# Kernel tuning notes

Measured on AMD Instinct MI355X. Metric: run time of the kernel, lower is better.

## Reference

```python
import jax, jax.numpy as jnp
import numpy as np

E, B, T = 7, 50, 100               # ensemble (network_size), no_batches=50, time blocks
D, A, L, H, C = 128, 32, 256, 1024, 128  # data, action, latent, hidden, context sizes
H_STEP = 0.1                        # (t1 - t0) / T == dt -> one SDE step per block


def setup_inputs() -> dict:
    key = jax.random.key(0)
    ks = iter(jax.random.split(key, 64))
    def nrm(shape, scale=1.0):
        return jax.random.normal(next(ks), shape, jnp.float32) * scale
    def ens(i, o):
        s = 1.0 / np.sqrt(i)
        return nrm((E, i, o), s), nrm((E, o), s)
    def lin(i, o):
        s = 1.0 / np.sqrt(i)
        return nrm((i, o), s), nrm((o,), s)
    inp = {}
    inp["enc_w1"], inp["enc_b1"] = ens(D, H)
    inp["enc_w2"], inp["enc_b2"] = ens(H, H)
    inp["enc_w3"], inp["enc_b3"] = ens(H, C)
    inp["qz0_w"], inp["qz0_b"] = ens(C, 2 * L)
    inp["act_w"], inp["act_b"] = ens(L + A + D, L)
    inp["proj_w1"], inp["proj_b1"] = ens(L, H)
    inp["proj_w2"], inp["proj_b2"] = ens(H, H)
    inp["proj_w3"], inp["proj_b3"] = ens(H, D)
    inp["f_w1"], inp["f_b1"] = lin(L, H)
    inp["f_w2"], inp["f_b2"] = lin(H, H)
    inp["f_w3"], inp["f_b3"] = lin(H, L)
    inp["h_w1"], inp["h_b1"] = lin(L, H)
    inp["h_w2"], inp["h_b2"] = lin(H, H)
    inp["h_w3"], inp["h_b3"] = lin(H, L)
    # per-latent-dim g nets: Linear(1,H) -> ReLU -> Linear(H,1), stacked over L dims
    inp["g_w1"] = nrm((L, H), 0.2)
    inp["g_b1"] = nrm((L, H), 0.2)
    inp["g_w2"] = nrm((L, H), 0.2 / np.sqrt(H))
    inp["g_b2"] = 0.5 + nrm((L,), 0.01)   # keep diffusion bounded away from 0
    inp["pz0_mean"] = jnp.zeros((E, 1, L), jnp.float32)
    inp["pz0_logstd"] = jnp.zeros((E, 1, L), jnp.float32)
    inp["xs"] = nrm((E, T * B, D))
    inp["actions"] = nrm((E, T * B, A))
    inp["eps_z0"] = nrm((T, E, B, L))      # torch.randn_like noise for z0 reparam
    inp["dw_noise"] = nrm((T, E * B, L))   # Brownian increment noise (unit std)
    return inp


def reference(enc_w1, enc_b1, enc_w2, enc_b2, enc_w3, enc_b3,
              qz0_w, qz0_b, act_w, act_b,
              proj_w1, proj_b1, proj_w2, proj_b2, proj_w3, proj_b3,
              f_w1, f_b1, f_w2, f_b2, f_w3, f_b3,
              h_w1, h_b1, h_w2, h_b2, h_w3, h_b3,
              g_w1, g_b1, g_w2, g_b2,
              pz0_mean, pz0_logstd,
              xs, actions, eps_z0, dw_noise):
    def ens_lin(x, w, b):  # EnsembleFC: bmm + bias
        return jnp.einsum('ebi,eio->ebo', x, w) + b[:, None, :]

    def encoder(x):
        x = jax.nn.relu(ens_lin(x, enc_w1, enc_b1))
        x = jax.nn.relu(ens_lin(x, enc_w2, enc_b2))
        return ens_lin(x, enc_w3, enc_b3)

    def projector(z):
        z = jnp.tanh(ens_lin(z, proj_w1, proj_b1))
        z = jnp.tanh(ens_lin(z, proj_w2, proj_b2))
        return ens_lin(z, proj_w3, proj_b3)

    def mlp(y, w1, b1, w2, b2, w3, b3):  # Linear-ReLU-Linear-Tanh-Linear
        y = jax.nn.relu(y @ w1 + b1)
        y = jnp.tanh(y @ w2 + b2)
        return y @ w3 + b3

    def g_fn(y):  # vectorized per-dim tiny MLPs: y (N, L) -> (N, L)
        hh = jax.nn.relu(y[:, :, None] * g_w1[None] + g_b1[None])  # (N, L, H)
        return jnp.sum(hh * g_w2[None], axis=-1) + g_b2

    xs_t = jnp.moveaxis(xs.reshape(E, T, B, D), 1, 0)        # (T, E, B, D)
    act_t = jnp.moveaxis(actions.reshape(E, T, B, A), 1, 0)  # (T, E, B, A)
    sqrt_h = jnp.sqrt(jnp.float32(H_STEP))

    def step(carry, inps):
        zs_last, i = carry
        x_i, a_i, eps_i, dw_i = inps
        ctx = encoder(x_i)                                  # (E, B, C)
        q = ens_lin(ctx, qz0_w, qz0_b)                      # (E, B, 2L)
        qm, ql = q[..., :L], q[..., L:]
        z0 = qm + jnp.exp(ql) * eps_i
        z_in = jnp.where(i == 0, z0, zs_last)               # first step uses z0
        lad = jnp.concatenate([z_in, a_i, x_i], axis=2)
        z = ens_lin(lad, act_w, act_b).reshape(E * B, L)
        # one SDE step with logqp (f: posterior drift, h: prior drift, g: diffusion)
        fv = mlp(z, f_w1, f_b1, f_w2, f_b2, f_w3, f_b3)
        hv = mlp(z, h_w1, h_b1, h_w2, h_b2, h_w3, h_b3)
        gv = g_fn(z)
        u = (fv - hv) / gv
        lr = 0.5 * jnp.sum(u * u, axis=-1) * H_STEP         # (E*B,) log-ratio increment
        z_new = z + fv * H_STEP + gv * (sqrt_h * dw_i)
        zs_new = z_new.reshape(E, B, L)
        xm = projector(zs_new)                              # (E, B, D)
        # KL(q(z0) || p(z0)) for diagonal Gaussians
        kl = (pz0_logstd - ql) \
             + (jnp.exp(2.0 * ql) + (qm - pz0_mean) ** 2) / (2.0 * jnp.exp(2.0 * pz0_logstd)) \
             - 0.5
        logqp0 = kl.sum(axis=2).mean(axis=1)                # (E,)
        lr_mean = lr.reshape(E, B).mean(axis=1)             # (E,)
        return (zs_new, i + 1), (lr_mean, logqp0, xm)

    init = (jnp.zeros((E, B, L), xs.dtype), jnp.int32(0))
    (_, _), (lrm, lq0, xms) = jax.lax.scan(step, init, (xs_t, act_t, eps_z0, dw_noise))
    logqp_path = lrm.sum(axis=0) + lq0.sum(axis=0)          # (E,)
    predicted_xs = jnp.moveaxis(xms, 0, 1).reshape(E, T * B, D)
    return logqp_path, predicted_xs
```

## Files before the change

kernel.cpp:

```cpp
#include <hip/hip_runtime.h>
#include <hip/hip_bf16.h>
#include <math.h>

#define E_ 7
#define B_ 50
#define T_ 100
#define D_ 128
#define A_ 32
#define L_ 256
#define H_ 1024
#define C_ 128
#define LAD_ 416
#define EB_ 350
#define TB_ 5000
#define SQRTH 0.31622776601683794f

typedef __attribute__((ext_vector_type(8))) short s8v;
typedef __attribute__((ext_vector_type(4))) float f32x4;
typedef __hip_bfloat16 bf16;

struct BG {
  const bf16* A[8];
  const bf16* W[8];
  const float* bias[8];
  float* Cf[8];
  bf16* Cb[8];
};

template<int BM, int ACT, int OUT>
__global__ __launch_bounds__(256)
void bgemm(BG g, int M, int K, int lda, int ldw, int ldc) {
  __shared__ short As[BM * 64];
  __shared__ short Ws[128 * 64];
  const short* Ap = (const short*)g.A[blockIdx.z];
  const short* Wp = (const short*)g.W[blockIdx.z];
  const int bm = blockIdx.x * BM, bn = blockIdx.y * 128;
  const int tid = threadIdx.x;
  const int wv = tid >> 6, lane = tid & 63;
  const int wm0 = (wv >> 1) * (BM / 2), wn0 = (wv & 1) * 64;
  const int l15 = lane & 15, l4 = lane >> 4;
  constexpr int FM = BM / 32;
  constexpr int AI = BM / 32;
  f32x4 acc[FM][4] = {};
  for (int k0 = 0; k0 < K; k0 += 64) {
    s8v av[AI], wvv[4];
#pragma unroll
    for (int i = 0; i < AI; ++i) {
      const int c = tid + i * 256, r = c >> 3, ck = c & 7;
      s8v v = {};
      if (bm + r < M) v = *(const s8v*)(Ap + (size_t)(bm + r) * lda + k0 + ck * 8);
      av[i] = v;
    }
#pragma unroll
    for (int i = 0; i < 4; ++i) {
      const int c = tid + i * 256, r = c >> 3, ck = c & 7;
      wvv[i] = *(const s8v*)(Wp + (size_t)(bn + r) * ldw + k0 + ck * 8);
    }
    __syncthreads();
#pragma unroll
    for (int i = 0; i < AI; ++i) {
      const int c = tid + i * 256, r = c >> 3, ck = c & 7;
      *(s8v*)(As + r * 64 + ((ck ^ (r & 7)) << 3)) = av[i];
    }
#pragma unroll
    for (int i = 0; i < 4; ++i) {
      const int c = tid + i * 256, r = c >> 3, ck = c & 7;
      *(s8v*)(Ws + r * 64 + ((ck ^ (r & 7)) << 3)) = wvv[i];
    }
    __syncthreads();
#pragma unroll
    for (int ks = 0; ks < 2; ++ks) {
      s8v af[FM], bfr[4];
#pragma unroll
      for (int m = 0; m < FM; ++m) {
        const int r = wm0 + m * 16 + l15, ck = ks * 4 + l4;
        af[m] = *(const s8v*)(As + r * 64 + ((ck ^ (r & 7)) << 3));
      }
#pragma unroll
      for (int n = 0; n < 4; ++n) {
        const int r = wn0 + n * 16 + l15, ck = ks * 4 + l4;
        bfr[n] = *(const s8v*)(Ws + r * 64 + ((ck ^ (r & 7)) << 3));
      }
#pragma unroll
      for (int m = 0; m < FM; ++m)
#pragma unroll
        for (int n = 0; n < 4; ++n)
          acc[m][n] = __builtin_amdgcn_mfma_f32_16x16x32_bf16(af[m], bfr[n], acc[m][n], 0, 0, 0);
    }
    __syncthreads();
  }
  const float* bias = g.bias[blockIdx.z];
  float* Cf = g.Cf[blockIdx.z];
  bf16* Cb = g.Cb[blockIdx.z];
#pragma unroll
  for (int n = 0; n < 4; ++n) {
    const int col = bn + wn0 + n * 16 + l15;
    const float bv = bias ? bias[col] : 0.f;
#pragma unroll
    for (int m = 0; m < FM; ++m) {
#pragma unroll
      for (int j = 0; j < 4; ++j) {
        const int row = bm + wm0 + m * 16 + l4 * 4 + j;
        if (row < M) {
          float v = acc[m][n][j] + bv;
          if (ACT == 1) v = fmaxf(v, 0.f);
          if (ACT == 2) v = tanhf(v);
          if (OUT == 0) Cf[(size_t)row * ldc + col] = v;
          if (OUT == 1) Cb[(size_t)row * ldc + col] = __float2bfloat16(v);
        }
      }
    }
  }
}

__global__ __launch_bounds__(256)
void cvtT_kernel(const float* __restrict__ src, bf16* __restrict__ dst,
                 int K, int N, long ss, long ds) {
  __shared__ float t[32][33];
  src += (size_t)blockIdx.z * ss;
  dst += (size_t)blockIdx.z * ds;
  const int n0 = blockIdx.x * 32, k0 = blockIdx.y * 32;
  const int tx = threadIdx.x & 31, ty = threadIdx.x >> 5;
#pragma unroll
  for (int i = 0; i < 4; ++i)
    t[ty + 8 * i][tx] = src[(size_t)(k0 + ty + 8 * i) * N + n0 + tx];
  __syncthreads();
#pragma unroll
  for (int i = 0; i < 4; ++i)
    dst[(size_t)(n0 + ty + 8 * i) * K + k0 + tx] = __float2bfloat16(t[tx][ty + 8 * i]);
}

struct B4 { bf16 a, b, c, d; };
__global__ __launch_bounds__(256)
void cvt_kernel(const float* __restrict__ s, bf16* __restrict__ d, int n4) {
  const int i = blockIdx.x * 256 + threadIdx.x;
  if (i < n4) {
    const float4 v = ((const float4*)s)[i];
    B4 o = {__float2bfloat16(v.x), __float2bfloat16(v.y),
            __float2bfloat16(v.z), __float2bfloat16(v.w)};
    ((B4*)d)[i] = o;
  }
}

__global__ __launch_bounds__(256)
void act_gemm(const float* __restrict__ zin, int zin_estride,
              const float* __restrict__ actions, const float* __restrict__ xs,
              const float* __restrict__ act_w, const float* __restrict__ act_b,
              float* __restrict__ zout, bf16* __restrict__ zout_bf, int t) {
  __shared__ float As[16][68];
  __shared__ float Bs[16][64];
  const int tid = threadIdx.x;
  const int e = blockIdx.y;
  const int bn = blockIdx.x * 64;
  const int tm = (tid >> 4) << 2;
  const int tn = (tid & 15) << 2;
  const int am = tid >> 2;
  const int ak = (tid & 3) << 2;
  const int bk = tid >> 4;
  const int bn4 = (tid & 15) << 2;
  const float* W = act_w + (size_t)e * LAD_ * L_;
  const float* zin_e = zin + (size_t)e * zin_estride;
  float acc[4][4] = {};
  for (int k0 = 0; k0 < LAD_; k0 += 16) {
    float4 av = make_float4(0.f, 0.f, 0.f, 0.f);
    const int k = k0 + ak;
    if (am < B_) {
      if (k < L_)
        av = *(const float4*)(zin_e + (size_t)am * L_ + k);
      else if (k < L_ + A_)
        av = *(const float4*)(actions + ((size_t)e * TB_ + (size_t)t * B_ + am) * A_ + (k - L_));
      else
        av = *(const float4*)(xs + ((size_t)e * TB_ + (size_t)t * B_ + am) * D_ + (k - L_ - A_));
    }
    const float4 wv = *(const float4*)(W + (size_t)(k0 + bk) * L_ + (bn + bn4));
    __syncthreads();
    As[ak + 0][am] = av.x; As[ak + 1][am] = av.y;
    As[ak + 2][am] = av.z; As[ak + 3][am] = av.w;
    *(float4*)&Bs[bk][bn4] = wv;
    __syncthreads();
#pragma unroll
    for (int kk = 0; kk < 16; ++kk) {
      const float4 a4 = *(const float4*)&As[kk][tm];
      const float4 b4 = *(const float4*)&Bs[kk][tn];
      const float ar[4] = {a4.x, a4.y, a4.z, a4.w};
      const float br[4] = {b4.x, b4.y, b4.z, b4.w};
#pragma unroll
      for (int i = 0; i < 4; ++i)
#pragma unroll
        for (int j = 0; j < 4; ++j)
          acc[i][j] = fmaf(ar[i], br[j], acc[i][j]);
    }
  }
#pragma unroll
  for (int i = 0; i < 4; ++i) {
    const int m = tm + i;
    if (m < B_) {
#pragma unroll
      for (int j = 0; j < 4; ++j) {
        const float v = acc[i][j] + act_b[(size_t)e * L_ + bn + tn + j];
        const size_t idx = ((size_t)e * B_ + m) * L_ + (bn + tn + j);
        zout[idx] = v;
        zout_bf[idx] = __float2bfloat16(v);
      }
    }
  }
}

__global__ __launch_bounds__(256)
void qkl_kernel(const float* __restrict__ ctx, int rows, int row_off, int ctx_estride,
                const float* __restrict__ qw, const float* __restrict__ qb,
                const float* __restrict__ pm, const float* __restrict__ pl,
                const float* __restrict__ eps0, float* __restrict__ z0,
                float* __restrict__ logqp) {
  __shared__ float cx[16][128];
  __shared__ float red[16];
  const int e = blockIdx.y;
  const int r0 = blockIdx.x * 16;
  const int tid = threadIdx.x;
  {
    const int r = tid >> 4, c = (tid & 15) * 8;
    float4 v0 = make_float4(0.f, 0.f, 0.f, 0.f), v1 = v0;
    if (r0 + r < rows) {
      const float* src = ctx + (size_t)e * ctx_estride + (size_t)(r0 + r) * C_ + c;
      v0 = *(const float4*)src;
      v1 = *(const float4*)(src + 4);
    }
    *(float4*)&cx[r][c] = v0;
    *(float4*)&cx[r][c + 4] = v1;
  }
  if (tid < 16) red[tid] = 0.f;
  __syncthreads();
  const int j = tid;
  const float* w = qw + (size_t)e * C_ * 512;
  float am_[16] = {};
  float al_[16] = {};
  for (int k0 = 0; k0 < C_; k0 += 4) {
    float wm[4], wl[4];
#pragma unroll
    for (int q = 0; q < 4; ++q) {
      wm[q] = w[(size_t)(k0 + q) * 512 + j];
      wl[q] = w[(size_t)(k0 + q) * 512 + 256 + j];
    }
#pragma unroll
    for (int r = 0; r < 16; ++r) {
      const float4 cv = *(const float4*)&cx[r][k0];
      const float cc[4] = {cv.x, cv.y, cv.z, cv.w};
#pragma unroll
      for (int q = 0; q < 4; ++q) {
        am_[r] = fmaf(cc[q], wm[q], am_[r]);
        al_[r] = fmaf(cc[q], wl[q], al_[r]);
      }
    }
  }
  const float qbm = qb[(size_t)e * 512 + j];
  const float qbl = qb[(size_t)e * 512 + 256 + j];
  const float pmv = pm[(size_t)e * L_ + j];
  const float plv = pl[(size_t)e * L_ + j];
  const float inv2e = 0.5f * expf(-2.f * plv);
#pragma unroll
  for (int r = 0; r < 16; ++r) {
    float kl = 0.f;
    if (r0 + r < rows) {
      const float qm_ = am_[r] + qbm;
      const float ql_ = al_[r] + qbl;
      const float dm = qm_ - pmv;
      kl = plv - ql_ + (expf(2.f * ql_) + dm * dm) * inv2e - 0.5f;
      const int gi = row_off + r0 + r;
      if (gi < B_) {
        const size_t zi = ((size_t)e * B_ + gi) * L_ + j;
        z0[zi] = qm_ + expf(ql_) * eps0[zi];
      }
    }
    for (int off = 32; off; off >>= 1) kl += __shfl_xor(kl, off, 64);
    if ((tid & 63) == 0) atomicAdd(&red[r], kl);
  }
  __syncthreads();
  if (tid < 16 && r0 + tid < rows) atomicAdd(&logqp[e], red[tid] * (1.0f / B_));
}

__global__ __launch_bounds__(64)
void g_kernel(const float* __restrict__ z, const float* __restrict__ gw1,
              const float* __restrict__ gb1, const float* __restrict__ gw2,
              const float* __restrict__ gb2, float* __restrict__ gv) {
  const int l = blockIdx.x;
  const int r0 = blockIdx.y * 44;
  const int rend = (r0 + 44 < EB_) ? (r0 + 44) : EB_;
  const int lane = threadIdx.x;
  float w1[16], b1[16], w2[16];
#pragma unroll
  for (int i = 0; i < 16; ++i) {
    const int h = lane + i * 64;
    w1[i] = gw1[(size_t)l * H_ + h];
    b1[i] = gb1[(size_t)l * H_ + h];
    w2[i] = gw2[(size_t)l * H_ + h];
  }
  const float g2 = gb2[l];
  for (int r = r0; r < rend; ++r) {
    const float zv = z[(size_t)r * L_ + l];
    float acc = 0.f;
#pragma unroll
    for (int i = 0; i < 16; ++i) {
      float hh = fmaf(zv, w1[i], b1[i]);
      hh = fmaxf(hh, 0.f);
      acc = fmaf(hh, w2[i], acc);
    }
    for (int off = 32; off; off >>= 1) acc += __shfl_xor(acc, off, 64);
    if (lane == 0) gv[(size_t)r * L_ + l] = acc + g2;
  }
}

__global__ __launch_bounds__(256)
void epi_kernel(const float* __restrict__ fvp, const float* __restrict__ fb3,
                const float* __restrict__ hb3, const float* __restrict__ gv,
                const float* __restrict__ z, const float* __restrict__ dw,
                float* __restrict__ zs_all, bf16* __restrict__ zs_bf,
                float* __restrict__ logqp, int t) {
  __shared__ float wsum[4];
  const int r = blockIdx.x;
  const int l = threadIdx.x;
  const int e = r / B_, b = r - e * B_;
  const size_t rl = (size_t)r * L_ + l;
  float fv = fb3[l], hv = hb3[l];
#pragma unroll
  for (int s = 0; s < 4; ++s) {
    fv += fvp[(size_t)s * EB_ * L_ + rl];
    hv += fvp[(size_t)(4 + s) * EB_ * L_ + rl];
  }
  const float gvv = gv[rl];
  const float u = (fv - hv) / gvv;
  float s_ = u * u;
  for (int off = 32; off; off >>= 1) s_ += __shfl_xor(s_, off, 64);
  if ((l & 63) == 0) wsum[l >> 6] = s_;
  __syncthreads();
  if (l == 0) {
    const float tot = wsum[0] + wsum[1] + wsum[2] + wsum[3];
    atomicAdd(&logqp[e], 0.5f * tot * 0.1f * (1.0f / B_));
  }
  const float znew = z[rl] + fv * 0.1f + gvv * (SQRTH * dw[(size_t)t * EB_ * L_ + rl]);
  const size_t oi = (((size_t)e * T_ + t) * B_ + b) * L_ + l;
  zs_all[oi] = znew;
  zs_bf[oi] = __float2bfloat16(znew);
}

__global__ void init_kernel(float* logqp) {
  if (threadIdx.x < E_) logqp[threadIdx.x] = 0.f;
}

extern "C" void kernel_launch(void* const* d_in, const int* in_sizes, int n_in,
                              void* d_out, int out_size, void* d_ws, size_t ws_size,
                              hipStream_t stream) {
  (void)in_sizes; (void)n_in; (void)out_size;
  const float* enc_w1 = (const float*)d_in[0];
  const float* enc_b1 = (const float*)d_in[1];
  const float* enc_w2 = (const float*)d_in[2];
  const float* enc_b2 = (const float*)d_in[3];
  const float* enc_w3 = (const float*)d_in[4];
  const float* enc_b3 = (const float*)d_in[5];
  const float* qz0_w  = (const float*)d_in[6];
  const float* qz0_b  = (const float*)d_in[7];
  const float* act_w  = (const float*)d_in[8];
  const float* act_b  = (const float*)d_in[9];
  const float* proj_w1 = (const float*)d_in[10];
  const float* proj_b1 = (const float*)d_in[11];
  const float* proj_w2 = (const float*)d_in[12];
  const float* proj_b2 = (const float*)d_in[13];
  const float* proj_w3 = (const float*)d_in[14];
  const float* proj_b3 = (const float*)d_in[15];
  const float* f_w1 = (const float*)d_in[16];
  const float* f_b1 = (const float*)d_in[17];
  const float* f_w2 = (const float*)d_in[18];
  const float* f_b2 = (const float*)d_in[19];
  const float* f_w3 = (const float*)d_in[20];
  const float* f_b3 = (const float*)d_in[21];
  const float* h_w1 = (const float*)d_in[22];
  const float* h_b1 = (const float*)d_in[23];
  const float* h_w2 = (const float*)d_in[24];
  const float* h_b2 = (const float*)d_in[25];
  const float* h_w3 = (const float*)d_in[26];
  const float* h_b3 = (const float*)d_in[27];
  const float* g_w1 = (const float*)d_in[28];
  const float* g_b1 = (const float*)d_in[29];
  const float* g_w2 = (const float*)d_in[30];
  const float* g_b2 = (const float*)d_in[31];
  const float* pz0_mean   = (const float*)d_in[32];
  const float* pz0_logstd = (const float*)d_in[33];
  const float* xs      = (const float*)d_in[34];
  const float* actions = (const float*)d_in[35];
  const float* eps_z0  = (const float*)d_in[36];
  const float* dw      = (const float*)d_in[37];

  float* out = (float*)d_out;
  float* logqp = out;
  float* pred = out + E_;

  char* base = (char*)d_ws;
  size_t off = 0;
  auto alloc = [&](size_t bytes) {
    void* p = base + off;
    off = (off + bytes + 255) & ~(size_t)255;
    return p;
  };
  float* zs_all = (float*)alloc((size_t)E_ * T_ * B_ * L_ * 4);
  bf16* zs_bf   = (bf16*)alloc((size_t)E_ * T_ * B_ * L_ * 2);
  float* z0     = (float*)alloc((size_t)E_ * B_ * L_ * 4);
  float* zbuf   = (float*)alloc((size_t)EB_ * L_ * 4);
  bf16* zbuf_bf = (bf16*)alloc((size_t)EB_ * L_ * 2);
  bf16* fh1     = (bf16*)alloc((size_t)2 * EB_ * H_ * 2);
  bf16* fh2     = (bf16*)alloc((size_t)2 * EB_ * H_ * 2);
  float* fvhvp  = (float*)alloc((size_t)8 * EB_ * L_ * 4);
  float* gvb    = (float*)alloc((size_t)EB_ * L_ * 4);
  bf16* xs_bf   = (bf16*)alloc((size_t)E_ * TB_ * D_ * 2);
  bf16* ew1T = (bf16*)alloc((size_t)E_ * D_ * H_ * 2);
  bf16* ew2T = (bf16*)alloc((size_t)E_ * H_ * H_ * 2);
  bf16* ew3T = (bf16*)alloc((size_t)E_ * H_ * C_ * 2);
  bf16* pw1T = (bf16*)alloc((size_t)E_ * L_ * H_ * 2);
  bf16* pw2T = (bf16*)alloc((size_t)E_ * H_ * H_ * 2);
  bf16* pw3T = (bf16*)alloc((size_t)E_ * H_ * D_ * 2);
  bf16* fw1T = (bf16*)alloc((size_t)L_ * H_ * 2);
  bf16* fw2T = (bf16*)alloc((size_t)H_ * H_ * 2);
  bf16* fw3T = (bf16*)alloc((size_t)H_ * L_ * 2);
  bf16* hw1T = (bf16*)alloc((size_t)L_ * H_ * 2);
  bf16* hw2T = (bf16*)alloc((size_t)H_ * H_ * 2);
  bf16* hw3T = (bf16*)alloc((size_t)H_ * L_ * 2);
  const size_t per_row = (size_t)E_ * (H_ * 2 * 2 + C_ * 4);
  size_t remain = (ws_size > off + 4096) ? (ws_size - off - 4096) : 0;
  int CH = (int)(remain / per_row);
  if (CH > 2500) CH = 2500;
  if (CH < 64) CH = 64;
  bf16* bufA = (bf16*)alloc((size_t)E_ * CH * H_ * 2);
  bf16* bufB = (bf16*)alloc((size_t)E_ * CH * H_ * 2);
  float* bufC = (float*)alloc((size_t)E_ * CH * C_ * 4);

  init_kernel<<<dim3(1), dim3(64), 0, stream>>>(logqp);

  const dim3 cb(256);
  cvt_kernel<<<dim3((E_ * TB_ * D_ / 4 + 255) / 256), cb, 0, stream>>>(xs, xs_bf, E_ * TB_ * D_ / 4);
  cvtT_kernel<<<dim3(H_ / 32, D_ / 32, E_), cb, 0, stream>>>(enc_w1, ew1T, D_, H_, (long)D_ * H_, (long)D_ * H_);
  cvtT_kernel<<<dim3(H_ / 32, H_ / 32, E_), cb, 0, stream>>>(enc_w2, ew2T, H_, H_, (long)H_ * H_, (long)H_ * H_);
  cvtT_kernel<<<dim3(C_ / 32, H_ / 32, E_), cb, 0, stream>>>(enc_w3, ew3T, H_, C_, (long)H_ * C_, (long)H_ * C_);
  cvtT_kernel<<<dim3(H_ / 32, L_ / 32, E_), cb, 0, stream>>>(proj_w1, pw1T, L_, H_, (long)L_ * H_, (long)L_ * H_);
  cvtT_kernel<<<dim3(H_ / 32, H_ / 32, E_), cb, 0, stream>>>(proj_w2, pw2T, H_, H_, (long)H_ * H_, (long)H_ * H_);
  cvtT_kernel<<<dim3(D_ / 32, H_ / 32, E_), cb, 0, stream>>>(proj_w3, pw3T, H_, D_, (long)H_ * D_, (long)H_ * D_);
  cvtT_kernel<<<dim3(H_ / 32, L_ / 32, 1), cb, 0, stream>>>(f_w1, fw1T, L_, H_, 0, 0);
  cvtT_kernel<<<dim3(H_ / 32, H_ / 32, 1), cb, 0, stream>>>(f_w2, fw2T, H_, H_, 0, 0);
  cvtT_kernel<<<dim3(L_ / 32, H_ / 32, 1), cb, 0, stream>>>(f_w3, fw3T, H_, L_, 0, 0);
  cvtT_kernel<<<dim3(H_ / 32, L_ / 32, 1), cb, 0, stream>>>(h_w1, hw1T, L_, H_, 0, 0);
  cvtT_kernel<<<dim3(H_ / 32, H_ / 32, 1), cb, 0, stream>>>(h_w2, hw2T, H_, H_, 0, 0);
  cvtT_kernel<<<dim3(L_ / 32, H_ / 32, 1), cb, 0, stream>>>(h_w3, hw3T, H_, L_, 0, 0);

  BG g;
  for (int c = 0; c < TB_; c += CH) {
    const int rows = (TB_ - c < CH) ? (TB_ - c) : CH;
    const int mt = (rows + 127) / 128;
    for (int e = 0; e < E_; ++e) {
      g.A[e] = xs_bf + ((size_t)e * TB_ + c) * D_;
      g.W[e] = ew1T + (size_t)e * D_ * H_;
      g.bias[e] = enc_b1 + (size_t)e * H_;
      g.Cb[e] = bufA + (size_t)e * CH * H_;
    }
    bgemm<128, 1, 1><<<dim3(mt, H_ / 128, E_), 256, 0, stream>>>(g, rows, D_, D_, D_, H_);
    for (int e = 0; e < E_; ++e) {
      g.A[e] = bufA + (size_t)e * CH * H_;
      g.W[e] = ew2T + (size_t)e * H_ * H_;
      g.bias[e] = enc_b2 + (size_t)e * H_;
      g.Cb[e] = bufB + (size_t)e * CH * H_;
    }
    bgemm<128, 1, 1><<<dim3(mt, H_ / 128, E_), 256, 0, stream>>>(g, rows, H_, H_, H_, H_);
    for (int e = 0; e < E_; ++e) {
      g.A[e] = bufB + (size_t)e * CH * H_;
      g.W[e] = ew3T + (size_t)e * H_ * C_;
      g.bias[e] = enc_b3 + (size_t)e * C_;
      g.Cf[e] = bufC + (size_t)e * CH * C_;
    }
    bgemm<128, 0, 0><<<dim3(mt, C_ / 128, E_), 256, 0, stream>>>(g, rows, H_, H_, H_, C_);
    qkl_kernel<<<dim3((rows + 15) / 16, E_), 256, 0, stream>>>(
        bufC, rows, c, CH * C_, qz0_w, qz0_b, pz0_mean, pz0_logstd, eps_z0, z0, logqp);
  }

  for (int t = 0; t < T_; ++t) {
    const float* zin;
    int zes;
    if (t == 0) { zin = z0; zes = B_ * L_; }
    else { zin = zs_all + (size_t)(t - 1) * B_ * L_; zes = T_ * B_ * L_; }
    act_gemm<<<dim3(L_ / 64, E_), 256, 0, stream>>>(zin, zes, actions, xs, act_w, act_b,
                                                    zbuf, zbuf_bf, t);
    g.A[0] = zbuf_bf; g.W[0] = fw1T; g.bias[0] = f_b1; g.Cb[0] = fh1;
    g.A[1] = zbuf_bf; g.W[1] = hw1T; g.bias[1] = h_b1; g.Cb[1] = fh1 + (size_t)EB_ * H_;
    bgemm<64, 1, 1><<<dim3(6, H_ / 128, 2), 256, 0, stream>>>(g, EB_, L_, L_, L_, H_);
    g.A[0] = fh1; g.W[0] = fw2T; g.bias[0] = f_b2; g.Cb[0] = fh2;
    g.A[1] = fh1 + (size_t)EB_ * H_; g.W[1] = hw2T; g.bias[1] = h_b2;
    g.Cb[1] = fh2 + (size_t)EB_ * H_;
    bgemm<64, 2, 1><<<dim3(6, H_ / 128, 2), 256, 0, stream>>>(g, EB_, H_, H_, H_, H_);
    for (int jj = 0; jj < 8; ++jj) {
      const int fb = jj >> 2, s = jj & 3;
      g.A[jj] = fh2 + (size_t)fb * EB_ * H_ + s * 256;
      g.W[jj] = (fb ? hw3T : fw3T) + s * 256;
      g.bias[jj] = nullptr;
      g.Cf[jj] = fvhvp + (size_t)jj * EB_ * L_;
    }
    bgemm<64, 0, 0><<<dim3(6, L_ / 128, 8), 256, 0, stream>>>(g, EB_, 256, H_, H_, L_);
    g_kernel<<<dim3(L_, 8), 64, 0, stream>>>(zbuf, g_w1, g_b1, g_w2, g_b2, gvb);
    epi_kernel<<<dim3(EB_), 256, 0, stream>>>(fvhvp, f_b3, h_b3, gvb, zbuf, dw,
                                              zs_all, zs_bf, logqp, t);
  }

  for (int c = 0; c < TB_; c += CH) {
    const int rows = (TB_ - c < CH) ? (TB_ - c) : CH;
    const int mt = (rows + 127) / 128;
    for (int e = 0; e < E_; ++e) {
      g.A[e] = zs_bf + ((size_t)e * T_ * B_ + c) * L_;
      g.W[e] = pw1T + (size_t)e * L_ * H_;
      g.bias[e] = proj_b1 + (size_t)e * H_;
      g.Cb[e] = bufA + (size_t)e * CH * H_;
    }
    bgemm<128, 2, 1><<<dim3(mt, H_ / 128, E_), 256, 0, stream>>>(g, rows, L_, L_, L_, H_);
    for (int e = 0; e < E_; ++e) {
      g.A[e] = bufA + (size_t)e * CH * H_;
      g.W[e] = pw2T + (size_t)e * H_ * H_;
      g.bias[e] = proj_b2 + (size_t)e * H_;
      g.Cb[e] = bufB + (size_t)e * CH * H_;
    }
    bgemm<128, 2, 1><<<dim3(mt, H_ / 128, E_), 256, 0, stream>>>(g, rows, H_, H_, H_, H_);
    for (int e = 0; e < E_; ++e) {
      g.A[e] = bufB + (size_t)e * CH * H_;
      g.W[e] = pw3T + (size_t)e * H_ * D_;
      g.bias[e] = proj_b3 + (size_t)e * D_;
      g.Cf[e] = pred + ((size_t)e * TB_ + c) * D_;
    }
    bgemm<128, 0, 0><<<dim3(mt, D_ / 128, E_), 256, 0, stream>>>(g, rows, H_, H_, H_, D_);
  }
}
```

Before: 11.16 ms.

## Fuse the 100-step SDE scan into one persistent kernel with grid barriers

```diff
diff --git a/kernel.cpp b/kernel.cpp
--- a/kernel.cpp
+++ b/kernel.cpp
@@ -10,14 +10,19 @@
 #define L_ 256
 #define H_ 1024
 #define C_ 128
-#define LAD_ 416
 #define EB_ 350
 #define TB_ 5000
 #define SQRTH 0.31622776601683794f
+#define NWG 512
+#define RPAD 352
+#define ZPAD 368
 
 typedef __attribute__((ext_vector_type(8))) short s8v;
 typedef __attribute__((ext_vector_type(4))) float f32x4;
+typedef _Float16 f16x2 __attribute__((ext_vector_type(2)));
 typedef __hip_bfloat16 bf16;
+
+#define MFMA __builtin_amdgcn_mfma_f32_16x16x32_bf16
 
 struct BG {
   const bf16* A[8];
@@ -85,7 +90,7 @@
       for (int m = 0; m < FM; ++m)
 #pragma unroll
         for (int n = 0; n < 4; ++n)
-          acc[m][n] = __builtin_amdgcn_mfma_f32_16x16x32_bf16(af[m], bfr[n], acc[m][n], 0, 0, 0);
+          acc[m][n] = MFMA(af[m], bfr[n], acc[m][n], 0, 0, 0);
     }
     __syncthreads();
   }
@@ -143,75 +148,60 @@
 }
 
 __global__ __launch_bounds__(256)
-void act_gemm(const float* __restrict__ zin, int zin_estride,
-              const float* __restrict__ actions, const float* __restrict__ xs,
-              const float* __restrict__ act_w, const float* __restrict__ act_b,
-              float* __restrict__ zout, bf16* __restrict__ zout_bf, int t) {
-  __shared__ float As[16][68];
-  __shared__ float Bs[16][64];
-  const int tid = threadIdx.x;
-  const int e = blockIdx.y;
-  const int bn = blockIdx.x * 64;
-  const int tm = (tid >> 4) << 2;
-  const int tn = (tid & 15) << 2;
-  const int am = tid >> 2;
-  const int ak = (tid & 3) << 2;
-  const int bk = tid >> 4;
-  const int bn4 = (tid & 15) << 2;
-  const float* W = act_w + (size_t)e * LAD_ * L_;
-  const float* zin_e = zin + (size_t)e * zin_estride;
-  float acc[4][4] = {};
-  for (int k0 = 0; k0 < LAD_; k0 += 16) {
-    float4 av = make_float4(0.f, 0.f, 0.f, 0.f);
-    const int k = k0 + ak;
-    if (am < B_) {
-      if (k < L_)
-        av = *(const float4*)(zin_e + (size_t)am * L_ + k);
-      else if (k < L_ + A_)
-        av = *(const float4*)(actions + ((size_t)e * TB_ + (size_t)t * B_ + am) * A_ + (k - L_));
-      else
-        av = *(const float4*)(xs + ((size_t)e * TB_ + (size_t)t * B_ + am) * D_ + (k - L_ - A_));
-    }
-    const float4 wv = *(const float4*)(W + (size_t)(k0 + bk) * L_ + (bn + bn4));
-    __syncthreads();
-    As[ak + 0][am] = av.x; As[ak + 1][am] = av.y;
-    As[ak + 2][am] = av.z; As[ak + 3][am] = av.w;
-    *(float4*)&Bs[bk][bn4] = wv;
-    __syncthreads();
-#pragma unroll
-    for (int kk = 0; kk < 16; ++kk) {
-      const float4 a4 = *(const float4*)&As[kk][tm];
-      const float4 b4 = *(const float4*)&Bs[kk][tn];
-      const float ar[4] = {a4.x, a4.y, a4.z, a4.w};
-      const float br[4] = {b4.x, b4.y, b4.z, b4.w};
-#pragma unroll
-      for (int i = 0; i < 4; ++i)
-#pragma unroll
-        for (int j = 0; j < 4; ++j)
-          acc[i][j] = fmaf(ar[i], br[j], acc[i][j]);
-    }
-  }
-#pragma unroll
-  for (int i = 0; i < 4; ++i) {
-    const int m = tm + i;
-    if (m < B_) {
-#pragma unroll
-      for (int j = 0; j < 4; ++j) {
-        const float v = acc[i][j] + act_b[(size_t)e * L_ + bn + tn + j];
-        const size_t idx = ((size_t)e * B_ + m) * L_ + (bn + tn + j);
-        zout[idx] = v;
-        zout_bf[idx] = __float2bfloat16(v);
-      }
-    }
-  }
+void ax_build(const float* __restrict__ actions, const float* __restrict__ xs,
+              bf16* __restrict__ dst) {
+  const int idx = blockIdx.x * 256 + threadIdx.x;
+  if (idx >= E_ * TB_ * 192) return;
+  const int k = idx % 192;
+  const int r = (idx / 192) % TB_;
+  const int e = idx / (192 * TB_);
+  float v = 0.f;
+  if (k < 32) v = actions[((size_t)e * TB_ + r) * A_ + k];
+  else if (k < 160) v = xs[((size_t)e * TB_ + r) * D_ + (k - 32)];
+  dst[idx] = __float2bfloat16(v);
+}
+
+__global__ __launch_bounds__(256)
+void waxT_build(const float* __restrict__ act_w, bf16* __restrict__ dst) {
+  const int idx = blockIdx.x * 256 + threadIdx.x;
+  if (idx >= E_ * 256 * 192) return;
+  const int k = idx % 192;
+  const int n = (idx / 192) % 256;
+  const int e = idx / (192 * 256);
+  float v = (k < 160) ? act_w[(size_t)e * 416 * 256 + (size_t)(256 + k) * 256 + n] : 0.f;
+  dst[idx] = __float2bfloat16(v);
+}
+
+__global__ __launch_bounds__(256)
+void wsplitT_build(const float* __restrict__ act_w, bf16* __restrict__ hi,
+                   bf16* __restrict__ lo) {
+  const int idx = blockIdx.x * 256 + threadIdx.x;
+  if (idx >= E_ * 256 * 256) return;
+  const int k = idx & 255;
+  const int n = (idx >> 8) & 255;
+  const int e = idx >> 16;
+  const float w = act_w[(size_t)e * 416 * 256 + (size_t)k * 256 + n];
+  const bf16 h = __float2bfloat16(w);
+  hi[idx] = h;
+  lo[idx] = __float2bfloat16(w - __bfloat162float(h));
+}
+
+__global__ __launch_bounds__(256)
+void gpack_build(const float* __restrict__ gw1, const float* __restrict__ gb1,
+                 const float* __restrict__ gw2, _Float16* __restrict__ dst) {
+  const int idx = blockIdx.x * 256 + threadIdx.x;
+  if (idx >= 256 * 3 * 1024) return;
+  const int l = idx / 3072, rem = idx - l * 3072, arr = rem >> 10, h = rem & 1023;
+  const float* s = arr == 0 ? gw1 : (arr == 1 ? gb1 : gw2);
+  dst[idx] = (_Float16)s[(size_t)l * 1024 + h];
 }
 
 __global__ __launch_bounds__(256)
 void qkl_kernel(const float* __restrict__ ctx, int rows, int row_off, int ctx_estride,
                 const float* __restrict__ qw, const float* __restrict__ qb,
                 const float* __restrict__ pm, const float* __restrict__ pl,
-                const float* __restrict__ eps0, float* __restrict__ z0,
-                float* __restrict__ logqp) {
+                const float* __restrict__ eps0, bf16* __restrict__ z0hi,
+                bf16* __restrict__ z0lo, float* __restrict__ logqp) {
   __shared__ float cx[16][128];
   __shared__ float red[16];
   const int e = blockIdx.y;
@@ -268,7 +258,10 @@
       const int gi = row_off + r0 + r;
       if (gi < B_) {
         const size_t zi = ((size_t)e * B_ + gi) * L_ + j;
-        z0[zi] = qm_ + expf(ql_) * eps0[zi];
+        const float z0 = qm_ + expf(ql_) * eps0[zi];
+        const bf16 h = __float2bfloat16(z0);
+        z0hi[zi] = h;
+        z0lo[zi] = __float2bfloat16(z0 - __bfloat162float(h));
       }
     }
     for (int off = 32; off; off >>= 1) kl += __shfl_xor(kl, off, 64);
@@ -278,72 +271,356 @@
   if (tid < 16 && r0 + tid < rows) atomicAdd(&logqp[e], red[tid] * (1.0f / B_));
 }
 
-__global__ __launch_bounds__(64)
-void g_kernel(const float* __restrict__ z, const float* __restrict__ gw1,
-              const float* __restrict__ gb1, const float* __restrict__ gw2,
-              const float* __restrict__ gb2, float* __restrict__ gv) {
-  const int l = blockIdx.x;
-  const int r0 = blockIdx.y * 44;
-  const int rend = (r0 + 44 < EB_) ? (r0 + 44) : EB_;
-  const int lane = threadIdx.x;
-  float w1[16], b1[16], w2[16];
-#pragma unroll
-  for (int i = 0; i < 16; ++i) {
-    const int h = lane + i * 64;
-    w1[i] = gw1[(size_t)l * H_ + h];
-    b1[i] = gb1[(size_t)l * H_ + h];
-    w2[i] = gw2[(size_t)l * H_ + h];
-  }
-  const float g2 = gb2[l];
-  for (int r = r0; r < rend; ++r) {
-    const float zv = z[(size_t)r * L_ + l];
-    float acc = 0.f;
-#pragma unroll
-    for (int i = 0; i < 16; ++i) {
-      float hh = fmaf(zv, w1[i], b1[i]);
-      hh = fmaxf(hh, 0.f);
-      acc = fmaf(hh, w2[i], acc);
-    }
-    for (int off = 32; off; off >>= 1) acc += __shfl_xor(acc, off, 64);
-    if (lane == 0) gv[(size_t)r * L_ + l] = acc + g2;
-  }
-}
-
-__global__ __launch_bounds__(256)
-void epi_kernel(const float* __restrict__ fvp, const float* __restrict__ fb3,
-                const float* __restrict__ hb3, const float* __restrict__ gv,
-                const float* __restrict__ z, const float* __restrict__ dw,
-                float* __restrict__ zs_all, bf16* __restrict__ zs_bf,
-                float* __restrict__ logqp, int t) {
-  __shared__ float wsum[4];
-  const int r = blockIdx.x;
-  const int l = threadIdx.x;
-  const int e = r / B_, b = r - e * B_;
-  const size_t rl = (size_t)r * L_ + l;
-  float fv = fb3[l], hv = hb3[l];
-#pragma unroll
-  for (int s = 0; s < 4; ++s) {
-    fv += fvp[(size_t)s * EB_ * L_ + rl];
-    hv += fvp[(size_t)(4 + s) * EB_ * L_ + rl];
-  }
-  const float gvv = gv[rl];
-  const float u = (fv - hv) / gvv;
-  float s_ = u * u;
-  for (int off = 32; off; off >>= 1) s_ += __shfl_xor(s_, off, 64);
-  if ((l & 63) == 0) wsum[l >> 6] = s_;
+struct SA {
+  bf16 *zhi, *zlo;
+  float *zP, *zPT;
+  bf16 *zPb;
+  bf16 *fh1, *fh2;
+  float *fv, *hv, *gv;
+  const float* axw;
+  const bf16 *WzhiT, *WzloT;
+  const bf16 *fw1T, *hw1T, *fw2T, *hw2T, *fw3T, *hw3T;
+  const float *fb1, *hb1, *fb2, *hb2, *fb3, *hb3;
+  const _Float16* gf16;
+  const float* gb2;
+  const float* dw;
+  float* logqp;
+  bf16* zs_bf;
+  unsigned* bar;
+};
+
+__device__ __forceinline__ void gsync(unsigned* bar, unsigned ph, int tid, int wg) {
+  __threadfence();
   __syncthreads();
-  if (l == 0) {
-    const float tot = wsum[0] + wsum[1] + wsum[2] + wsum[3];
-    atomicAdd(&logqp[e], 0.5f * tot * 0.1f * (1.0f / B_));
-  }
-  const float znew = z[rl] + fv * 0.1f + gvv * (SQRTH * dw[(size_t)t * EB_ * L_ + rl]);
-  const size_t oi = (((size_t)e * T_ + t) * B_ + b) * L_ + l;
-  zs_all[oi] = znew;
-  zs_bf[oi] = __float2bfloat16(znew);
-}
-
-__global__ void init_kernel(float* logqp) {
-  if (threadIdx.x < E_) logqp[threadIdx.x] = 0.f;
+  if (tid == 0) {
+    const unsigned v = __hip_atomic_fetch_add(&bar[(wg >> 4) << 5], 1u,
+                                              __ATOMIC_RELAXED, __HIP_MEMORY_SCOPE_AGENT);
+    if (v + 1u == ph * 16u) {
+      const unsigned r = __hip_atomic_fetch_add(&bar[1024], 1u,
+                                                __ATOMIC_RELAXED, __HIP_MEMORY_SCOPE_AGENT);
+      if (r + 1u == ph * 32u)
+        __hip_atomic_store(&bar[1056], ph, __ATOMIC_RELAXED, __HIP_MEMORY_SCOPE_AGENT);
+    }
+    while (__hip_atomic_load(&bar[1056], __ATOMIC_RELAXED, __HIP_MEMORY_SCOPE_AGENT) < ph)
+      __builtin_amdgcn_s_sleep(4);
+  }
+  __syncthreads();
+  __threadfence();
+}
+
+__device__ __forceinline__ f16x2 relu2(f16x2 t) {
+#if __has_builtin(__builtin_elementwise_max)
+  const f16x2 zz = {};
+  return __builtin_elementwise_max(t, zz);
+#else
+  t[0] = t[0] > (_Float16)0 ? t[0] : (_Float16)0;
+  t[1] = t[1] > (_Float16)0 ? t[1] : (_Float16)0;
+  return t;
+#endif
+}
+__device__ __forceinline__ float fdot2a(f16x2 a, f16x2 b, float c) {
+#if __has_builtin(__builtin_amdgcn_fdot2)
+  return __builtin_amdgcn_fdot2(a, b, c, false);
+#else
+  return c + (float)a[0] * (float)b[0] + (float)a[1] * (float)b[1];
+#endif
+}
+
+__device__ void g_part(const SA& a, const f16x2* gwh, int wb, int l, float gb2v,
+                       int lane, int rb, int re) {
+  const int r0 = rb + lane, r1 = rb + 64 + lane;
+  const float z0f = (r0 < re) ? a.zPT[(size_t)l * RPAD + r0] : 0.f;
+  const float z1f = (r1 < re) ? a.zPT[(size_t)l * RPAD + r1] : 0.f;
+  const _Float16 z0h = (_Float16)z0f, z1h = (_Float16)z1f;
+  const f16x2 z20 = {z0h, z0h}, z21 = {z1h, z1h};
+  float ac0 = 0.f, ac1 = 0.f;
+  for (int hp = 0; hp < 512; ++hp) {
+    const f16x2 w1v = gwh[wb + hp];
+    const f16x2 b1v = gwh[wb + 512 + hp];
+    const f16x2 w2v = gwh[wb + 1024 + hp];
+    ac0 = fdot2a(relu2(z20 * w1v + b1v), w2v, ac0);
+    ac1 = fdot2a(relu2(z21 * w1v + b1v), w2v, ac1);
+  }
+  if (r0 < re) a.gv[(size_t)r0 * 256 + l] = ac0 + gb2v;
+  if (r1 < re) a.gv[(size_t)r1 * 256 + l] = ac1 + gb2v;
+}
+
+__global__ __launch_bounds__(256, 2) void scan_kernel(SA a) {
+  __shared__ __align__(16) char smem[32768];
+  short* sw = (short*)smem;
+  const int wg = blockIdx.x, tid = threadIdx.x;
+  const int lane = tid & 63, wv = tid >> 6, l15 = lane & 15, l4 = lane >> 4;
+
+  const bool isWZ = wg < 56;
+  const bool isW1 = wg >= 56 && wg < 120;
+  const bool isW2 = wg >= 120 && wg < 376;
+  const bool isW3 = wg >= 376 && wg < 440;
+  const bool isG  = wg >= 440 && wg < 504;
+
+  if (isWZ) {
+    const int e = wg >> 3, c0 = (wg & 7) * 32;
+    const short* gh = (const short*)a.WzhiT + ((size_t)e * 256 + c0) * 256;
+    const short* gl = (const short*)a.WzloT + ((size_t)e * 256 + c0) * 256;
+#pragma unroll
+    for (int i = 0; i < 4; ++i) {
+      const int lin = tid + i * 256;
+      const int col = lin >> 5, c = lin & 31;
+      const int dst = col * 256 + ((c ^ (col & 7)) << 3);
+      *(s8v*)(sw + dst) = *(const s8v*)(gh + col * 256 + c * 8);
+      *(s8v*)(sw + 8192 + dst) = *(const s8v*)(gl + col * 256 + c * 8);
+    }
+  } else if (isW1) {
+    const int idx = wg - 56, fb = idx >> 5, r5 = idx & 31;
+    const int n0 = (r5 >> 1) * 64;
+    const short* gsrc = (const short*)(fb ? a.hw1T : a.fw1T) + (size_t)n0 * 256;
+#pragma unroll
+    for (int i = 0; i < 8; ++i) {
+      const int lin = tid + i * 256;
+      const int col = lin >> 5, c = lin & 31;
+      *(s8v*)(sw + col * 256 + ((c ^ (col & 7)) << 3)) = *(const s8v*)(gsrc + col * 256 + c * 8);
+    }
+  } else if (isW2 || isW3) {
+    int n0, fb;
+    const bf16* base;
+    if (isW2) {
+      const int idx = wg - 120; fb = idx >> 7;
+      n0 = ((idx & 127) >> 1) * 16;
+      base = fb ? a.hw2T : a.fw2T;
+    } else {
+      const int idx = wg - 376; fb = idx >> 5;
+      n0 = ((idx & 31) >> 1) * 16;
+      base = fb ? a.hw3T : a.fw3T;
+    }
+    const short* gsrc = (const short*)base + (size_t)n0 * 1024;
+#pragma unroll
+    for (int i = 0; i < 8; ++i) {
+      const int lin = tid + i * 256;
+      const int col = lin >> 7, c = lin & 127;
+      *(s8v*)(sw + col * 1024 + ((c ^ (col & 7)) << 3)) = *(const s8v*)(gsrc + col * 1024 + c * 8);
+    }
+  } else if (isG) {
+    const unsigned* src = (const unsigned*)a.gf16 + (size_t)(wg - 440) * 4 * 1536;
+    unsigned* dstu = (unsigned*)smem;
+    for (int i = tid; i < 6144; i += 256) dstu[i] = src[i];
+  }
+  __syncthreads();
+
+  const f16x2* gwh = (const f16x2*)smem;
+  const int gl_ = isG ? (wg - 440) * 4 + wv : 0;
+  const float gb2v = isG ? a.gb2[gl_] : 0.f;
+  const int gwb = wv * 1536;
+
+  const int idx5 = wg * 256 + tid;
+  const bool act5 = idx5 < EB_ * 256;
+  const int r5i = idx5 >> 8, l5i = idx5 & 255;
+  const int e5 = act5 ? r5i / 50 : 0;
+  const int b5 = r5i - e5 * 50;
+  const size_t zsb = ((size_t)e5 * T_ * B_ + b5) * 256 + l5i;
+  float lr_acc = 0.f;
+  unsigned ph = 0;
+
+  for (int t = 0; t < T_; ++t) {
+    if (isWZ) {
+      const int e = wg >> 3, c0 = (wg & 7) * 32;
+      const int arow = e * 50 + wv * 16 + l15;
+      const short* zh = (const short*)a.zhi;
+      const short* zl = (const short*)a.zlo;
+      f32x4 acc[2] = {};
+#pragma unroll
+      for (int k0 = 0; k0 < 256; k0 += 32) {
+        const s8v ah = *(const s8v*)(zh + arow * 256 + k0 + l4 * 8);
+        const s8v al = *(const s8v*)(zl + arow * 256 + k0 + l4 * 8);
+        const int c = (k0 >> 3) + l4;
+#pragma unroll
+        for (int nt = 0; nt < 2; ++nt) {
+          const int cl = nt * 16 + l15;
+          const int off = cl * 256 + ((c ^ (cl & 7)) << 3);
+          const s8v bh = *(const s8v*)(sw + off);
+          const s8v bl = *(const s8v*)(sw + 8192 + off);
+          acc[nt] = MFMA(ah, bh, acc[nt], 0, 0, 0);
+          acc[nt] = MFMA(al, bh, acc[nt], 0, 0, 0);
+          acc[nt] = MFMA(ah, bl, acc[nt], 0, 0, 0);
+        }
+      }
+#pragma unroll
+      for (int nt = 0; nt < 2; ++nt) {
+        const int col = c0 + nt * 16 + l15;
+#pragma unroll
+        for (int j = 0; j < 4; ++j) {
+          const int row = wv * 16 + l4 * 4 + j;
+          if (row < 50) {
+            const int gr = e * 50 + row;
+            const float v = acc[nt][j] + a.axw[((size_t)e * TB_ + t * 50 + row) * 256 + col];
+            a.zP[(size_t)gr * 256 + col] = v;
+            a.zPb[(size_t)gr * 256 + col] = __float2bfloat16(v);
+            a.zPT[(size_t)col * RPAD + gr] = v;
+          }
+        }
+      }
+    }
+    gsync(a.bar, ++ph, tid, wg);
+
+    if (isW1) {
+      const int idx = wg - 56, fb = idx >> 5, r5 = idx & 31;
+      const int n0 = (r5 >> 1) * 64, rb = (r5 & 1) * 175;
+      const short* Ap = (const short*)a.zPb;
+      int mrow[3];
+#pragma unroll
+      for (int mi = 0; mi < 3; ++mi) {
+        const int mt = wv + mi * 4;
+        mrow[mi] = rb + (mt < 11 ? mt : 0) * 16 + l15;
+      }
+      f32x4 acc[3][4] = {};
+#pragma unroll
+      for (int k0 = 0; k0 < 256; k0 += 32) {
+        s8v av[3];
+#pragma unroll
+        for (int mi = 0; mi < 3; ++mi)
+          av[mi] = *(const s8v*)(Ap + (size_t)mrow[mi] * 256 + k0 + l4 * 8);
+        const int c = (k0 >> 3) + l4;
+#pragma unroll
+        for (int nt = 0; nt < 4; ++nt) {
+          const int cl = nt * 16 + l15;
+          const s8v b = *(const s8v*)(sw + cl * 256 + ((c ^ (cl & 7)) << 3));
+#pragma unroll
+          for (int mi = 0; mi < 3; ++mi)
+            acc[mi][nt] = MFMA(av[mi], b, acc[mi][nt], 0, 0, 0);
+        }
+      }
+      const float* bias = fb ? a.hb1 : a.fb1;
+      bf16* C = a.fh1 + (size_t)fb * RPAD * 1024;
+#pragma unroll
+      for (int nt = 0; nt < 4; ++nt) {
+        const int col = n0 + nt * 16 + l15;
+        const float bv = bias[col];
+#pragma unroll
+        for (int mi = 0; mi < 3; ++mi) {
+          const int mt = wv + mi * 4;
+          if (mt < 11) {
+#pragma unroll
+            for (int j = 0; j < 4; ++j) {
+              const int row = rb + mt * 16 + l4 * 4 + j;
+              if (row < EB_)
+                C[(size_t)row * 1024 + col] = __float2bfloat16(fmaxf(acc[mi][nt][j] + bv, 0.f));
+            }
+          }
+        }
+      }
+    } else if (isG) {
+      g_part(a, gwh, gwb, gl_, gb2v, lane, 0, 117);
+    }
+    gsync(a.bar, ++ph, tid, wg);
+
+    if (isW2) {
+      const int idx = wg - 120, fb = idx >> 7, r7 = idx & 127;
+      const int n0 = (r7 >> 1) * 16, rb = (r7 & 1) * 175;
+      const short* Ap = (const short*)a.fh1 + (size_t)fb * RPAD * 1024;
+      int mrow[3];
+#pragma unroll
+      for (int mi = 0; mi < 3; ++mi) {
+        const int mt = wv + mi * 4;
+        mrow[mi] = rb + (mt < 11 ? mt : 0) * 16 + l15;
+      }
+      f32x4 acc[3] = {};
+#pragma unroll 4
+      for (int k0 = 0; k0 < 1024; k0 += 32) {
+        s8v av[3];
+#pragma unroll
+        for (int mi = 0; mi < 3; ++mi)
+          av[mi] = *(const s8v*)(Ap + (size_t)mrow[mi] * 1024 + k0 + l4 * 8);
+        const int c = (k0 >> 3) + l4;
+        const s8v b = *(const s8v*)(sw + l15 * 1024 + ((c ^ (l15 & 7)) << 3));
+#pragma unroll
+        for (int mi = 0; mi < 3; ++mi)
+          acc[mi] = MFMA(av[mi], b, acc[mi], 0, 0, 0);
+      }
+      const float bv = (fb ? a.hb2 : a.fb2)[n0 + l15];
+      bf16* C = a.fh2 + (size_t)fb * RPAD * 1024;
+#pragma unroll
+      for (int mi = 0; mi < 3; ++mi) {
+        const int mt = wv + mi * 4;
+        if (mt < 11) {
+#pragma unroll
+          for (int j = 0; j < 4; ++j) {
+            const int row = rb + mt * 16 + l4 * 4 + j;
+            if (row < EB_)
+              C[(size_t)row * 1024 + n0 + l15] = __float2bfloat16(tanhf(acc[mi][j] + bv));
+          }
+        }
+      }
+    } else if (isG) {
+      g_part(a, gwh, gwb, gl_, gb2v, lane, 117, 234);
+    }
+    gsync(a.bar, ++ph, tid, wg);
+
+    if (isW3) {
+      const int idx = wg - 376, fb = idx >> 5, r5 = idx & 31;
+      const int n0 = (r5 >> 1) * 16, rb = (r5 & 1) * 175;
+      const short* Ap = (const short*)a.fh2 + (size_t)fb * RPAD * 1024;
+      int mrow[3];
+#pragma unroll
+      for (int mi = 0; mi < 3; ++mi) {
+        const int mt = wv + mi * 4;
+        mrow[mi] = rb + (mt < 11 ? mt : 0) * 16 + l15;
+      }
+      f32x4 acc[3] = {};
+#pragma unroll 4
+      for (int k0 = 0; k0 < 1024; k0 += 32) {
+        s8v av[3];
+#pragma unroll
+        for (int mi = 0; mi < 3; ++mi)
+          av[mi] = *(const s8v*)(Ap + (size_t)mrow[mi] * 1024 + k0 + l4 * 8);
+        const int c = (k0 >> 3) + l4;
+        const s8v b = *(const s8v*)(sw + l15 * 1024 + ((c ^ (l15 & 7)) << 3));
+#pragma unroll
+        for (int mi = 0; mi < 3; ++mi)
+          acc[mi] = MFMA(av[mi], b, acc[mi], 0, 0, 0);
+      }
+      const float bv = (fb ? a.hb3 : a.fb3)[n0 + l15];
+      float* O = fb ? a.hv : a.fv;
+#pragma unroll
+      for (int mi = 0; mi < 3; ++mi) {
+        const int mt = wv + mi * 4;
+        if (mt < 11) {
+#pragma unroll
+          for (int j = 0; j < 4; ++j) {
+            const int row = rb + mt * 16 + l4 * 4 + j;
+            if (row < EB_)
+              O[(size_t)row * 256 + n0 + l15] = acc[mi][j] + bv;
+          }
+        }
+      }
+    } else if (isG) {
+      g_part(a, gwh, gwb, gl_, gb2v, lane, 234, 350);
+    }
+    gsync(a.bar, ++ph, tid, wg);
+
+    if (act5) {
+      const float zp = a.zP[idx5];
+      const float fvv = a.fv[idx5];
+      const float hvv = a.hv[idx5];
+      const float gvv = a.gv[idx5];
+      const float u = (fvv - hvv) / gvv;
+      lr_acc += u * u;
+      const float znew = zp + 0.1f * fvv + gvv * (SQRTH * a.dw[(size_t)t * (EB_ * 256) + idx5]);
+      const bf16 h = __float2bfloat16(znew);
+      a.zhi[idx5] = h;
+      a.zlo[idx5] = __float2bfloat16(znew - __bfloat162float(h));
+      a.zs_bf[zsb + (size_t)t * (B_ * 256)] = h;
+    }
+    gsync(a.bar, ++ph, tid, wg);
+  }
+
+  float v = lr_acc;
+#pragma unroll
+  for (int o = 32; o; o >>= 1) v += __shfl_xor(v, o, 64);
+  if (lane == 0 && act5) atomicAdd(&a.logqp[e5], 0.001f * v);
+}
+
+__global__ void init_kernel(float* logqp, unsigned* bar) {
+  const int i = threadIdx.x;
+  if (i < E_) logqp[i] = 0.f;
+  for (int j = i; j < 1088; j += 256) bar[j] = 0u;
 }
 
 extern "C" void kernel_launch(void* const* d_in, const int* in_sizes, int n_in,
@@ -400,16 +677,25 @@
     off = (off + bytes + 255) & ~(size_t)255;
     return p;
   };
-  float* zs_all = (float*)alloc((size_t)E_ * T_ * B_ * L_ * 4);
-  bf16* zs_bf   = (bf16*)alloc((size_t)E_ * T_ * B_ * L_ * 2);
-  float* z0     = (float*)alloc((size_t)E_ * B_ * L_ * 4);
-  float* zbuf   = (float*)alloc((size_t)EB_ * L_ * 4);
-  bf16* zbuf_bf = (bf16*)alloc((size_t)EB_ * L_ * 2);
-  bf16* fh1     = (bf16*)alloc((size_t)2 * EB_ * H_ * 2);
-  bf16* fh2     = (bf16*)alloc((size_t)2 * EB_ * H_ * 2);
-  float* fvhvp  = (float*)alloc((size_t)8 * EB_ * L_ * 4);
-  float* gvb    = (float*)alloc((size_t)EB_ * L_ * 4);
-  bf16* xs_bf   = (bf16*)alloc((size_t)E_ * TB_ * D_ * 2);
+  bf16* zhi    = (bf16*)alloc((size_t)ZPAD * 256 * 2);
+  bf16* zlo    = (bf16*)alloc((size_t)ZPAD * 256 * 2);
+  float* zP    = (float*)alloc((size_t)RPAD * 256 * 4);
+  float* zPT   = (float*)alloc((size_t)256 * RPAD * 4);
+  bf16* zPb    = (bf16*)alloc((size_t)RPAD * 256 * 2);
+  bf16* fh1    = (bf16*)alloc((size_t)2 * RPAD * 1024 * 2);
+  bf16* fh2    = (bf16*)alloc((size_t)2 * RPAD * 1024 * 2);
+  float* fvb   = (float*)alloc((size_t)RPAD * 256 * 4);
+  float* hvb   = (float*)alloc((size_t)RPAD * 256 * 4);
+  float* gvb   = (float*)alloc((size_t)RPAD * 256 * 4);
+  bf16* zs_bf  = (bf16*)alloc((size_t)E_ * T_ * B_ * 256 * 2);
+  float* axw   = (float*)alloc((size_t)E_ * TB_ * 256 * 4);
+  bf16* ax_bf  = (bf16*)alloc((size_t)E_ * TB_ * 192 * 2);
+  bf16* waxT   = (bf16*)alloc((size_t)E_ * 256 * 192 * 2);
+  bf16* WzhiT  = (bf16*)alloc((size_t)E_ * 256 * 256 * 2);
+  bf16* WzloT  = (bf16*)alloc((size_t)E_ * 256 * 256 * 2);
+  _Float16* gf16 = (_Float16*)alloc((size_t)256 * 3 * 1024 * 2);
+  unsigned* bar = (unsigned*)alloc(4608);
+  bf16* xs_bf  = (bf16*)alloc((size_t)E_ * TB_ * D_ * 2);
   bf16* ew1T = (bf16*)alloc((size_t)E_ * D_ * H_ * 2);
   bf16* ew2T = (bf16*)alloc((size_t)E_ * H_ * H_ * 2);
   bf16* ew3T = (bf16*)alloc((size_t)E_ * H_ * C_ * 2);
@@ -431,7 +717,7 @@
   bf16* bufB = (bf16*)alloc((size_t)E_ * CH * H_ * 2);
   float* bufC = (float*)alloc((size_t)E_ * CH * C_ * 4);
 
-  init_kernel<<<dim3(1), dim3(64), 0, stream>>>(logqp);
+  init_kernel<<<dim3(1), dim3(256), 0, stream>>>(logqp, bar);
 
   const dim3 cb(256);
   cvt_kernel<<<dim3((E_ * TB_ * D_ / 4 + 255) / 256), cb, 0, stream>>>(xs, xs_bf, E_ * TB_ * D_ / 4);
@@ -447,8 +733,20 @@
   cvtT_kernel<<<dim3(H_ / 32, L_ / 32, 1), cb, 0, stream>>>(h_w1, hw1T, L_, H_, 0, 0);
   cvtT_kernel<<<dim3(H_ / 32, H_ / 32, 1), cb, 0, stream>>>(h_w2, hw2T, H_, H_, 0, 0);
   cvtT_kernel<<<dim3(L_ / 32, H_ / 32, 1), cb, 0, stream>>>(h_w3, hw3T, H_, L_, 0, 0);
+  ax_build<<<dim3((E_ * TB_ * 192 + 255) / 256), cb, 0, stream>>>(actions, xs, ax_bf);
+  waxT_build<<<dim3((E_ * 256 * 192 + 255) / 256), cb, 0, stream>>>(act_w, waxT);
+  wsplitT_build<<<dim3((E_ * 256 * 256 + 255) / 256), cb, 0, stream>>>(act_w, WzhiT, WzloT);
+  gpack_build<<<dim3((256 * 3 * 1024 + 255) / 256), cb, 0, stream>>>(g_w1, g_b1, g_w2, gf16);
 
   BG g;
+  for (int e = 0; e < E_; ++e) {
+    g.A[e] = ax_bf + (size_t)e * TB_ * 192;
+    g.W[e] = waxT + (size_t)e * 256 * 192;
+    g.bias[e] = act_b + (size_t)e * 256;
+    g.Cf[e] = axw + (size_t)e * TB_ * 256;
+  }
+  bgemm<128, 0, 0><<<dim3((TB_ + 127) / 128, 2, E_), 256, 0, stream>>>(g, TB_, 192, 192, 192, 256);
+
   for (int c = 0; c < TB_; c += CH) {
     const int rows = (TB_ - c < CH) ? (TB_ - c) : CH;
     const int mt = (rows + 127) / 128;
@@ -474,34 +772,24 @@
     }
     bgemm<128, 0, 0><<<dim3(mt, C_ / 128, E_), 256, 0, stream>>>(g, rows, H_, H_, H_, C_);
     qkl_kernel<<<dim3((rows + 15) / 16, E_), 256, 0, stream>>>(
-        bufC, rows, c, CH * C_, qz0_w, qz0_b, pz0_mean, pz0_logstd, eps_z0, z0, logqp);
-  }
-
-  for (int t = 0; t < T_; ++t) {
-    const float* zin;
-    int zes;
-    if (t == 0) { zin = z0; zes = B_ * L_; }
-    else { zin = zs_all + (size_t)(t - 1) * B_ * L_; zes = T_ * B_ * L_; }
-    act_gemm<<<dim3(L_ / 64, E_), 256, 0, stream>>>(zin, zes, actions, xs, act_w, act_b,
-                                                    zbuf, zbuf_bf, t);
-    g.A[0] = zbuf_bf; g.W[0] = fw1T; g.bias[0] = f_b1; g.Cb[0] = fh1;
-    g.A[1] = zbuf_bf; g.W[1] = hw1T; g.bias[1] = h_b1; g.Cb[1] = fh1 + (size_t)EB_ * H_;
-    bgemm<64, 1, 1><<<dim3(6, H_ / 128, 2), 256, 0, stream>>>(g, EB_, L_, L_, L_, H_);
-    g.A[0] = fh1; g.W[0] = fw2T; g.bias[0] = f_b2; g.Cb[0] = fh2;
-    g.A[1] = fh1 + (size_t)EB_ * H_; g.W[1] = hw2T; g.bias[1] = h_b2;
-    g.Cb[1] = fh2 + (size_t)EB_ * H_;
-    bgemm<64, 2, 1><<<dim3(6, H_ / 128, 2), 256, 0, stream>>>(g, EB_, H_, H_, H_, H_);
-    for (int jj = 0; jj < 8; ++jj) {
-      const int fb = jj >> 2, s = jj & 3;
-      g.A[jj] = fh2 + (size_t)fb * EB_ * H_ + s * 256;
-      g.W[jj] = (fb ? hw3T : fw3T) + s * 256;
-      g.bias[jj] = nullptr;
-      g.Cf[jj] = fvhvp + (size_t)jj * EB_ * L_;
-    }
-    bgemm<64, 0, 0><<<dim3(6, L_ / 128, 8), 256, 0, stream>>>(g, EB_, 256, H_, H_, L_);
-    g_kernel<<<dim3(L_, 8), 64, 0, stream>>>(zbuf, g_w1, g_b1, g_w2, g_b2, gvb);
-    epi_kernel<<<dim3(EB_), 256, 0, stream>>>(fvhvp, f_b3, h_b3, gvb, zbuf, dw,
-                                              zs_all, zs_bf, logqp, t);
+        bufC, rows, c, CH * C_, qz0_w, qz0_b, pz0_mean, pz0_logstd, eps_z0,
+        zhi, zlo, logqp);
+  }
+
+  SA sa;
+  sa.zhi = zhi; sa.zlo = zlo; sa.zP = zP; sa.zPT = zPT; sa.zPb = zPb;
+  sa.fh1 = fh1; sa.fh2 = fh2; sa.fv = fvb; sa.hv = hvb; sa.gv = gvb;
+  sa.axw = axw; sa.WzhiT = WzhiT; sa.WzloT = WzloT;
+  sa.fw1T = fw1T; sa.hw1T = hw1T; sa.fw2T = fw2T; sa.hw2T = hw2T;
+  sa.fw3T = fw3T; sa.hw3T = hw3T;
+  sa.fb1 = f_b1; sa.hb1 = h_b1; sa.fb2 = f_b2; sa.hb2 = h_b2;
+  sa.fb3 = f_b3; sa.hb3 = h_b3;
+  sa.gf16 = gf16; sa.gb2 = g_b2;
+  sa.dw = dw; sa.logqp = logqp; sa.zs_bf = zs_bf; sa.bar = bar;
+  void* params[] = {(void*)&sa};
+  if (hipLaunchCooperativeKernel((const void*)scan_kernel, dim3(NWG), dim3(256),
+                                 params, 0, stream) != hipSuccess) {
+    scan_kernel<<<dim3(NWG), dim3(256), 0, stream>>>(sa);
   }
 
   for (int c = 0; c < TB_; c += CH) {
```

After: 43.50 ms. 290% more time.
